# Kernel tuning notes

Hardware: AMD Instinct MI355X
Metric: run time of the kernel (lower is better)

## Reference

```python
import jax, jax.numpy as jnp
import numpy as np

NUM_CLASSES = 20
NUM_ANCHORS = 3
BBOX_ATTRS = 5 + NUM_CLASSES
IMG_H = IMG_W = 416
IN_H = IN_W = 52
CONF_THRES = 0.5
NMS_THRES = 0.4
TOP_K = 2048


def setup_inputs() -> dict:
    key = jax.random.key(0)
    k1, _ = jax.random.split(key)
    inp = jax.random.normal(k1, (16, NUM_ANCHORS * BBOX_ATTRS, IN_H, IN_W), dtype=jnp.float32)
    anchors = jnp.array([[116.0, 90.0], [156.0, 198.0], [373.0, 326.0]], dtype=jnp.float32)
    return {"input": inp, "anchors": anchors}


def decode(inp, anchors):
    """YOLOv3 head decode (YOLOv3Loss.forward with targets=None).
    inp: [B, A*(5+C), H, W] -> output: [B, A*H*W, 5+C] with (cx, cy, w, h, conf, cls...)."""
    bs = inp.shape[0]
    stride_h = IMG_H / IN_H
    stride_w = IMG_W / IN_W
    scaled_anchors = anchors / jnp.array([stride_w, stride_h], dtype=inp.dtype)  # [A, 2]
    # [B, A, H, W, 5+C]
    pred = inp.reshape(bs, NUM_ANCHORS, BBOX_ATTRS, IN_H, IN_W).transpose(0, 1, 3, 4, 2)
    x = jax.nn.sigmoid(pred[..., 0])
    y = jax.nn.sigmoid(pred[..., 1])
    w = pred[..., 2]
    h = pred[..., 3]
    conf = jax.nn.sigmoid(pred[..., 4])
    pred_cls = jax.nn.sigmoid(pred[..., 5:])
    grid_x = jnp.arange(IN_W, dtype=inp.dtype)[None, None, None, :]
    grid_y = jnp.arange(IN_H, dtype=inp.dtype)[None, None, :, None]
    anchor_w = scaled_anchors[:, 0][None, :, None, None]
    anchor_h = scaled_anchors[:, 1][None, :, None, None]
    bx = (x + grid_x) * stride_w
    by = (y + grid_y) * stride_h
    bw = jnp.exp(w) * anchor_w * stride_w
    bh = jnp.exp(h) * anchor_h * stride_h
    boxes = jnp.stack([bx, by, bw, bh], axis=-1).reshape(bs, -1, 4)
    output = jnp.concatenate(
        [boxes, conf.reshape(bs, -1, 1), pred_cls.reshape(bs, -1, NUM_CLASSES)], axis=-1
    )
    return output


def _nms_one(corners, conf, cls_pred):
    """Greedy class-aware NMS over TOP_K conf-sorted candidates.
    corners: [K,4] x1y1x2y2, conf: [K] desc-sorted, cls_pred: [K] int32.
    Returns keep mask [K] bool."""
    x1, y1, x2, y2 = corners[:, 0], corners[:, 1], corners[:, 2], corners[:, 3]
    area = (x2 - x1 + 1.0) * (y2 - y1 + 1.0)
    ix1 = jnp.maximum(x1[:, None], x1[None, :])
    iy1 = jnp.maximum(y1[:, None], y1[None, :])
    ix2 = jnp.minimum(x2[:, None], x2[None, :])
    iy2 = jnp.minimum(y2[:, None], y2[None, :])
    inter = jnp.clip(ix2 - ix1 + 1.0, 0.0) * jnp.clip(iy2 - iy1 + 1.0, 0.0)
    iou = inter / (area[:, None] + area[None, :] - inter + 1e-16)
    # suppress j if kept i (earlier, higher conf, same class) overlaps >= thres
    cond = (iou >= NMS_THRES) & (cls_pred[:, None] == cls_pred[None, :])
    valid = conf >= CONF_THRES
    K = conf.shape[0]
    idx = jnp.arange(K)

    def body(i, carry):
        keep, supp = carry
        ki = valid[i] & (~supp[i])
        keep = keep.at[i].set(ki)
        supp = supp | (cond[i] & (idx > i) & ki)
        return keep, supp

    keep, _ = jax.lax.fori_loop(0, K, body, (jnp.zeros(K, bool), jnp.zeros(K, bool)))
    return keep


def reference(input, anchors):
    output = decode(input, anchors)  # [B, N, 5+C]
    conf = output[..., 4]
    # top-K candidates by objectness (desc order == conf sort in original NMS)
    top_conf, top_idx = jax.lax.top_k(conf, TOP_K)  # [B, K]
    boxes = output[..., :4]
    cx, cy, w, h = boxes[..., 0], boxes[..., 1], boxes[..., 2], boxes[..., 3]
    corners = jnp.stack([cx - w / 2, cy - h / 2, cx + w / 2, cy + h / 2], axis=-1)
    corners_s = jnp.take_along_axis(corners, top_idx[..., None], axis=1)  # [B, K, 4]
    cls_pred = jnp.argmax(output[..., 5:], axis=-1).astype(jnp.int32)  # [B, N]
    cls_s = jnp.take_along_axis(cls_pred, top_idx, axis=1)  # [B, K]
    keep = jax.vmap(_nms_one)(corners_s, top_conf, cls_s)  # [B, K] bool
    return output, top_idx, keep
```

## Files before the change

kernel.cpp:

```cpp
#include <hip/hip_runtime.h>

#pragma clang fp contract(off)

#define B 16
#define A 3
#define HGT 52
#define WID 52
#define HW 2704
#define NCAND 8112
#define CATTR 25
#define TOPK 2048
#define NWORD 64
#define CH 128
#define NCHUNK (TOPK / CH)
#define EPT 8

typedef unsigned int uint32;
typedef unsigned long long u64;

__global__ void decode_kernel(const float* __restrict__ inp,
                              const float* __restrict__ anchors,
                              float* __restrict__ out,
                              float* __restrict__ cws) {
    int t = blockIdx.x * blockDim.x + threadIdx.x;
    if (t >= B * NCAND) return;
    int b  = t / NCAND;
    int n  = t - b * NCAND;
    int a  = n / HW;
    int hw = n - a * HW;
    int gy = hw / WID;
    int gx = hw - gy * WID;
    const float* ip = inp + ((size_t)(b * (A * CATTR) + a * CATTR)) * HW + hw;
    float* op = out + (size_t)t * CATTR;

    float p0 = ip[0 * HW], p1 = ip[1 * HW], p2 = ip[2 * HW], p3 = ip[3 * HW], p4 = ip[4 * HW];
    float sx = 1.0f / (1.0f + expf(-p0));
    float sy = 1.0f / (1.0f + expf(-p1));
    float bx = (sx + (float)gx) * 8.0f;
    float by = (sy + (float)gy) * 8.0f;
    float bw = expf(p2) * anchors[a * 2 + 0];
    float bh = expf(p3) * anchors[a * 2 + 1];
    float cf = 1.0f / (1.0f + expf(-p4));
    op[0] = bx; op[1] = by; op[2] = bw; op[3] = bh; op[4] = cf;
    cws[t] = cf;
#pragma unroll
    for (int c = 0; c < 20; ++c) {
        float v = ip[(5 + c) * HW];
        op[5 + c] = 1.0f / (1.0f + expf(-v));
    }
}

__device__ __forceinline__ void cexd(u64& a, u64& b, bool up) {
    if ((a > b) == up) { u64 tmp = a; a = b; b = tmp; }
}

__device__ __forceinline__ u64 sel(u64 k, u64 o, bool kmin) {
    return kmin ? (k < o ? k : o) : (k > o ? k : o);
}

__device__ __forceinline__ void bitonic_merge_2048(u64 key[EPT], u64* mb, int t) {
    for (unsigned j = 1024; j >= 8; j >>= 1) {
        unsigned m = j >> 3;
        bool kmin = ((t & m) == 0);
        if (m >= 64) {
            __syncthreads();
#pragma unroll
            for (int e = 0; e < EPT; ++e) mb[e * 256 + t] = key[e];
            __syncthreads();
            int pt = t ^ (int)m;
#pragma unroll
            for (int e = 0; e < EPT; ++e) key[e] = sel(key[e], mb[e * 256 + pt], kmin);
        } else {
#pragma unroll
            for (int e = 0; e < EPT; ++e) {
                u64 o = __shfl_xor(key[e], (int)m);
                key[e] = sel(key[e], o, kmin);
            }
        }
    }
    cexd(key[0], key[4], true); cexd(key[1], key[5], true);
    cexd(key[2], key[6], true); cexd(key[3], key[7], true);
    cexd(key[0], key[2], true); cexd(key[1], key[3], true);
    cexd(key[4], key[6], true); cexd(key[5], key[7], true);
    cexd(key[0], key[1], true); cexd(key[2], key[3], true);
    cexd(key[4], key[5], true); cexd(key[6], key[7], true);
}

__global__ __launch_bounds__(256) void sort1_kernel(const float* __restrict__ conf,
                                                    u64* __restrict__ runs) {
    __shared__ u64 mb[2048];
    int blk = blockIdx.x;
    int b = blk >> 2, c = blk & 3;
    int t = threadIdx.x;
    int base = t * EPT;
    int gbase = c * 2048 + base;
    const float* cp = conf + b * NCAND;

    u64 key[EPT];
    if (gbase + EPT <= NCAND) {
        const float4* cp4 = (const float4*)(cp + gbase);
        float4 c0 = cp4[0], c1 = cp4[1];
        float cf[EPT] = {c0.x, c0.y, c0.z, c0.w, c1.x, c1.y, c1.z, c1.w};
#pragma unroll
        for (int e = 0; e < EPT; ++e) {
            unsigned bits = __float_as_uint(cf[e]) | 0x80000000u;
            key[e] = ((u64)(~bits) << 32) | (unsigned)(gbase + e);
        }
    } else {
#pragma unroll
        for (int e = 0; e < EPT; ++e) {
            int idx = gbase + e;
            if (idx < NCAND) {
                unsigned bits = __float_as_uint(cp[idx]) | 0x80000000u;
                key[e] = ((u64)(~bits) << 32) | (unsigned)idx;
            } else key[e] = ~0ull;
        }
    }

    cexd(key[0], key[1], true); cexd(key[2], key[3], false);
    cexd(key[4], key[5], true); cexd(key[6], key[7], false);

    cexd(key[0], key[2], true);  cexd(key[1], key[3], true);
    cexd(key[4], key[6], false); cexd(key[5], key[7], false);
    cexd(key[0], key[1], true);  cexd(key[2], key[3], true);
    cexd(key[4], key[5], false); cexd(key[6], key[7], false);

    bool up8 = ((t & 1) == 0);
    cexd(key[0], key[4], up8); cexd(key[1], key[5], up8);
    cexd(key[2], key[6], up8); cexd(key[3], key[7], up8);
    cexd(key[0], key[2], up8); cexd(key[1], key[3], up8);
    cexd(key[4], key[6], up8); cexd(key[5], key[7], up8);
    cexd(key[0], key[1], up8); cexd(key[2], key[3], up8);
    cexd(key[4], key[5], up8); cexd(key[6], key[7], up8);

    for (unsigned k = 16; k <= 2048; k <<= 1) {
        bool up = (((unsigned)base & k) == 0);
        for (unsigned j = k >> 1; j >= 8; j >>= 1) {
            unsigned m = j >> 3;
            bool kmin = (up == ((t & m) == 0));
            if (m >= 64) {
                __syncthreads();
#pragma unroll
                for (int e = 0; e < EPT; ++e) mb[e * 256 + t] = key[e];
                __syncthreads();
                int pt = t ^ (int)m;
#pragma unroll
                for (int e = 0; e < EPT; ++e) key[e] = sel(key[e], mb[e * 256 + pt], kmin);
            } else {
#pragma unroll
                for (int e = 0; e < EPT; ++e) {
                    u64 o = __shfl_xor(key[e], (int)m);
                    key[e] = sel(key[e], o, kmin);
                }
            }
        }
        cexd(key[0], key[4], up); cexd(key[1], key[5], up);
        cexd(key[2], key[6], up); cexd(key[3], key[7], up);
        cexd(key[0], key[2], up); cexd(key[1], key[3], up);
        cexd(key[4], key[6], up); cexd(key[5], key[7], up);
        cexd(key[0], key[1], up); cexd(key[2], key[3], up);
        cexd(key[4], key[5], up); cexd(key[6], key[7], up);
    }

    u64* R = runs + ((size_t)b * 4 + c) * 2048;
#pragma unroll
    for (int e = 0; e < EPT; ++e) R[base + e] = key[e];
}

__global__ __launch_bounds__(256) void sort2_kernel(const u64* __restrict__ runs,
                                                    u64* __restrict__ half) {
    __shared__ u64 mb[2048];
    int blk = blockIdx.x;
    int b = blk >> 1, p = blk & 1;
    int t = threadIdx.x;
    int base = t * EPT;
    const u64* Av = runs + ((size_t)b * 4 + p * 2) * 2048;
    const u64* Bv = Av + 2048;

    u64 key[EPT];
#pragma unroll
    for (int e = 0; e < EPT; ++e) {
        u64 a = Av[base + e];
        u64 o = Bv[2047 - (base + e)];
        key[e] = a < o ? a : o;
    }
    bitonic_merge_2048(key, mb, t);
    u64* H = half + ((size_t)b * 2 + p) * 2048;
#pragma unroll
    for (int e = 0; e < EPT; ++e) H[base + e] = key[e];
}

__global__ __launch_bounds__(256) void sort3_kernel(const u64* __restrict__ half,
                                                    float* __restrict__ topf) {
    __shared__ u64 mb[2048];
    int b = blockIdx.x;
    int t = threadIdx.x;
    int base = t * EPT;
    const u64* Av = half + (size_t)b * 2 * 2048;
    const u64* Bv = Av + 2048;

    u64 key[EPT];
#pragma unroll
    for (int e = 0; e < EPT; ++e) {
        u64 a = Av[base + e];
        u64 o = Bv[2047 - (base + e)];
        key[e] = a < o ? a : o;
    }
    bitonic_merge_2048(key, mb, t);
#pragma unroll
    for (int e = 0; e < EPT; ++e)
        topf[(size_t)b * TOPK + base + e] = (float)(unsigned)(key[e] & 0xFFFFFFFFu);
}

__global__ __launch_bounds__(256) void geo_kernel(const float* __restrict__ out,
                                                  const float* __restrict__ topf,
                                                  float* __restrict__ gx1,
                                                  float* __restrict__ gy1,
                                                  float* __restrict__ gx2,
                                                  float* __restrict__ gy2,
                                                  float* __restrict__ gar,
                                                  uint32* __restrict__ gcv,
                                                  uint32* __restrict__ vwords) {
    int t = blockIdx.x * blockDim.x + threadIdx.x;
    if (t >= B * TOPK) return;
    int b = t >> 11;
    int r = t & (TOPK - 1);
    int idx = (int)topf[(size_t)b * TOPK + r];
    const float* p = out + ((size_t)b * NCAND + idx) * CATTR;
    float cx = p[0], cy = p[1], w = p[2], h = p[3], cf = p[4];
    float hw_ = w * 0.5f, hh_ = h * 0.5f;
    float x1 = cx - hw_, y1 = cy - hh_, x2 = cx + hw_, y2 = cy + hh_;
    gx1[t] = x1; gy1[t] = y1; gx2[t] = x2; gy2[t] = y2;
    gar[t] = ((x2 - x1) + 1.0f) * ((y2 - y1) + 1.0f);
    float best = p[5]; int bc = 0;
#pragma unroll
    for (int c = 1; c < 20; ++c) {
        float v = p[5 + c];
        if (v > best) { best = v; bc = c; }
    }
    bool valid = (cf >= 0.5f);
    gcv[t] = (uint32)bc | (valid ? 0x100u : 0u);
    unsigned long long bal = __ballot(valid);
    if ((t & 63) == 0) {
        vwords[(t >> 5) + 0] = (uint32)bal;
        vwords[(t >> 5) + 1] = (uint32)(bal >> 32);
    }
}

#define KMID (13421772.5 / 33554432.0)
__global__ __launch_bounds__(1024) void build_kernel(const float* __restrict__ gx1,
                                                     const float* __restrict__ gy1,
                                                     const float* __restrict__ gx2,
                                                     const float* __restrict__ gy2,
                                                     const float* __restrict__ gar,
                                                     const uint32* __restrict__ gcv,
                                                     uint32* __restrict__ rowmask) {
    __shared__ float4 x4s[TOPK];
    __shared__ float  ars[TOPK];
    __shared__ uint32 clss[TOPK];
    int bt   = blockIdx.y;
    int pr   = blockIdx.x;
    int tid  = threadIdx.x;
    int lane = tid & 63;
    int wvq  = tid >> 6;
    int base = bt * TOPK;
    u64* rm64 = (u64*)(rowmask + (size_t)base * NWORD);

    for (int j = tid; j < TOPK; j += 1024) {
        int g = base + j;
        x4s[j]  = make_float4(gx1[g], gy1[g], gx2[g], gy2[g]);
        ars[j]  = gar[g];
        clss[j] = gcv[g] & 0xffu;
    }
    __syncthreads();

#pragma unroll
    for (int s = 0; s < 2; ++s) {
        int r = s ? (31 - pr) : pr;
        int i0 = r * 64 + wvq * 4;
        float4 rq[4]; float rar4[4]; uint32 rcl4[4];
#pragma unroll
        for (int k = 0; k < 4; ++k) {
            rq[k] = x4s[i0 + k]; rar4[k] = ars[i0 + k]; rcl4[k] = clss[i0 + k];
        }
        for (int cg = r; cg < 32; ++cg) {
            int j = cg * 64 + lane;
            float4 c  = x4s[j];
            float car = ars[j];
            uint32 cc = clss[j];
            u64 bal[4];
#pragma unroll
            for (int k = 0; k < 4; ++k) {
                float ix1 = fmaxf(rq[k].x, c.x);
                float iy1 = fmaxf(rq[k].y, c.y);
                float ix2 = fminf(rq[k].z, c.z);
                float iy2 = fminf(rq[k].w, c.w);
                float iw = fmaxf((ix2 - ix1) + 1.0f, 0.0f);
                float ih = fmaxf((iy2 - iy1) + 1.0f, 0.0f);
                float inter = iw * ih;
                float denom = ((rar4[k] + car) - inter) + 1e-16f;
                bool cond = ((double)inter > KMID * (double)denom) && (cc == rcl4[k]);
                bal[k] = __ballot(cond);
            }
            u64 v = bal[0];
            if (lane == 1) v = bal[1];
            if (lane == 2) v = bal[2];
            if (lane == 3) v = bal[3];
            if (lane < 4) rm64[(size_t)(i0 + lane) * 32 + cg] = v;
        }
    }
}

#define SPF 8
__global__ __launch_bounds__(1024) void scan_kernel(const uint32* __restrict__ rowmask,
                                                    const uint32* __restrict__ vwords,
                                                    float* __restrict__ keepf) {
    __shared__ uint32 buf[2][CH * NWORD];
    int bt  = blockIdx.x;
    int tid = threadIdx.x;
    int wv  = tid >> 6;
    int l   = tid & 63;
    const uint32* rm = rowmask + (size_t)bt * TOPK * NWORD;

    if (wv > 0) {
        int ctid = tid - 64;
        const uint4* src = (const uint4*)rm;
        uint4* dst = (uint4*)buf[0];
        for (int o = ctid; o < CH * NWORD / 4; o += 960) dst[o] = src[o];
    }
    uint32 vw = 0, supp = 0, keepw = 0, cur = 0, vcur = 0;
    if (wv == 0) vw = vwords[bt * 64 + l];
    __syncthreads();

    for (int c = 0; c < NCHUNK; ++c) {
        if (wv > 0) {
            if (c + 1 < NCHUNK) {
                int ctid = tid - 64;
                const uint4* src = (const uint4*)(rm + (size_t)(c + 1) * CH * NWORD);
                uint4* dst = (uint4*)buf[(c + 1) & 1];
                for (int o = ctid; o < CH * NWORD / 4; o += 960) dst[o] = src[o];
            }
        } else {
            const uint32* bp = buf[c & 1];
            uint32 rlb[SPF], rwb[SPF];
#pragma unroll
            for (int k = 0; k < SPF; ++k) {
                rlb[k] = bp[k * NWORD + l];
                rwb[k] = bp[k * NWORD + ((c * CH + k) >> 5)];
            }
            for (int kk = 0; kk < CH; kk += SPF) {
#pragma unroll
                for (int k2 = 0; k2 < SPF; ++k2) {
                    int k = kk + k2;
                    int i = c * CH + k;
                    uint32 rl = rlb[k2], rw = rwb[k2];
                    int nk = k + SPF;
                    if (nk < CH) {
                        rlb[k2] = bp[nk * NWORD + l];
                        rwb[k2] = bp[nk * NWORD + ((c * CH + nk) >> 5)];
                    }
                    int b2 = i & 31;
                    if (b2 == 0) {
                        cur  = __shfl(supp, i >> 5);
                        vcur = __shfl(vw,   i >> 5);
                    }
                    uint32 kf = ((vcur >> b2) & ~(cur >> b2)) & 1u;
                    uint32 m = (uint32)(-(int)kf);
                    cur  |= rw & m;
                    supp |= rl & m;
                    if (l == (i >> 5)) keepw |= kf << b2;
                }
            }
        }
        __syncthreads();
    }

    if (wv == 0) {
#pragma unroll
        for (int k = 0; k < 32; ++k)
            keepf[bt * TOPK + l * 32 + k] = (float)((keepw >> k) & 1u);
    }
}

extern "C" void kernel_launch(void* const* d_in, const int* in_sizes, int n_in,
                              void* d_out, int out_size, void* d_ws, size_t ws_size,
                              hipStream_t stream) {
    const float* inp     = (const float*)d_in[0];
    const float* anchors = (const float*)d_in[1];
    float* out   = (float*)d_out;
    float* topf  = out  + (size_t)B * NCAND * CATTR;
    float* keepf = topf + (size_t)B * TOPK;

    float*  cws = (float*)d_ws;
    float*  gx1 = cws + B * NCAND;
    float*  gy1 = gx1 + B * TOPK;
    float*  gx2 = gy1 + B * TOPK;
    float*  gy2 = gx2 + B * TOPK;
    float*  gar = gy2 + B * TOPK;
    uint32* gcv = (uint32*)(gar + B * TOPK);
    uint32* rowmask = gcv + B * TOPK;
    uint32* vwords  = rowmask + (size_t)B * TOPK * NWORD;
    u64* runs = (u64*)rowmask;
    u64* half = runs + (size_t)B * 4 * 2048;

    int total = B * NCAND;
    decode_kernel<<<(total + 255) / 256, 256, 0, stream>>>(inp, anchors, out, cws);
    sort1_kernel<<<B * 4, 256, 0, stream>>>(cws, runs);
    sort2_kernel<<<B * 2, 256, 0, stream>>>(runs, half);
    sort3_kernel<<<B, 256, 0, stream>>>(half, topf);
    geo_kernel<<<(B * TOPK + 255) / 256, 256, 0, stream>>>(out, topf, gx1, gy1, gx2, gy2, gar, gcv, vwords);
    build_kernel<<<dim3(16, B), 1024, 0, stream>>>(gx1, gy1, gx2, gy2, gar, gcv, rowmask);
    scan_kernel<<<B, 1024, 0, stream>>>(rowmask, vwords, keepf);
}
```

Measured before the change: 206.5 us.

## Coalesce decode stores via LDS, fuse geo into sort3, restructure NMS scan

The decode kernel stages each block's 25-attribute rows in shared memory and writes them out as coalesced float4 stores instead of strided per-thread stores. The geometry/class gather is folded into the final sort merge kernel, which removes one launch and the topf round-trip. The NMS scan now resolves 32 candidates at a time within a word using a register-resident diagonal, then ORs in the suppression rows of kept boxes only. This replaces the per-row serial shuffle loop, with a larger chunk size. Fusing geo into sort3 leaves only 16 blocks doing the gathers, so that work runs with much less parallelism than before.

Measured after the change: 257.3 us. +24.6%, slower.

```diff
diff --git a/kernel.cpp b/kernel.cpp
--- a/kernel.cpp
+++ b/kernel.cpp
@@ -11,19 +11,21 @@
 #define CATTR 25
 #define TOPK 2048
 #define NWORD 64
-#define CH 128
+#define CH 256
 #define NCHUNK (TOPK / CH)
+#define GPC (CH / 32)
 #define EPT 8
 
 typedef unsigned int uint32;
 typedef unsigned long long u64;
 
-__global__ void decode_kernel(const float* __restrict__ inp,
-                              const float* __restrict__ anchors,
-                              float* __restrict__ out,
-                              float* __restrict__ cws) {
-    int t = blockIdx.x * blockDim.x + threadIdx.x;
-    if (t >= B * NCAND) return;
+__global__ __launch_bounds__(256) void decode_kernel(const float* __restrict__ inp,
+                                                     const float* __restrict__ anchors,
+                                                     float* __restrict__ out,
+                                                     float* __restrict__ cws) {
+    __shared__ float sm[256 * CATTR];
+    int tid = threadIdx.x;
+    int t = blockIdx.x * 256 + tid;
     int b  = t / NCAND;
     int n  = t - b * NCAND;
     int a  = n / HW;
@@ -31,7 +33,7 @@
     int gy = hw / WID;
     int gx = hw - gy * WID;
     const float* ip = inp + ((size_t)(b * (A * CATTR) + a * CATTR)) * HW + hw;
-    float* op = out + (size_t)t * CATTR;
+    float* sp = sm + tid * CATTR;
 
     float p0 = ip[0 * HW], p1 = ip[1 * HW], p2 = ip[2 * HW], p3 = ip[3 * HW], p4 = ip[4 * HW];
     float sx = 1.0f / (1.0f + expf(-p0));
@@ -41,13 +43,19 @@
     float bw = expf(p2) * anchors[a * 2 + 0];
     float bh = expf(p3) * anchors[a * 2 + 1];
     float cf = 1.0f / (1.0f + expf(-p4));
-    op[0] = bx; op[1] = by; op[2] = bw; op[3] = bh; op[4] = cf;
+    sp[0] = bx; sp[1] = by; sp[2] = bw; sp[3] = bh; sp[4] = cf;
     cws[t] = cf;
 #pragma unroll
     for (int c = 0; c < 20; ++c) {
         float v = ip[(5 + c) * HW];
-        op[5 + c] = 1.0f / (1.0f + expf(-v));
-    }
+        sp[5 + c] = 1.0f / (1.0f + expf(-v));
+    }
+    __syncthreads();
+    const float4* sm4 = (const float4*)sm;
+    float4* o4 = (float4*)(out + (size_t)blockIdx.x * 256 * CATTR);
+#pragma unroll
+    for (int k = 0; k < 6; ++k) o4[k * 256 + tid] = sm4[k * 256 + tid];
+    if (tid < 64) o4[1536 + tid] = sm4[1536 + tid];
 }
 
 __device__ __forceinline__ void cexd(u64& a, u64& b, bool up) {
@@ -191,8 +199,17 @@
 }
 
 __global__ __launch_bounds__(256) void sort3_kernel(const u64* __restrict__ half,
-                                                    float* __restrict__ topf) {
+                                                    const float* __restrict__ out,
+                                                    float* __restrict__ topf,
+                                                    float* __restrict__ gx1,
+                                                    float* __restrict__ gy1,
+                                                    float* __restrict__ gx2,
+                                                    float* __restrict__ gy2,
+                                                    float* __restrict__ gar,
+                                                    uint32* __restrict__ gcv,
+                                                    uint32* __restrict__ vwords) {
     __shared__ u64 mb[2048];
+    __shared__ uint32 vb[256];
     int b = blockIdx.x;
     int t = threadIdx.x;
     int base = t * EPT;
@@ -207,43 +224,34 @@
         key[e] = a < o ? a : o;
     }
     bitonic_merge_2048(key, mb, t);
-#pragma unroll
-    for (int e = 0; e < EPT; ++e)
-        topf[(size_t)b * TOPK + base + e] = (float)(unsigned)(key[e] & 0xFFFFFFFFu);
-}
-
-__global__ __launch_bounds__(256) void geo_kernel(const float* __restrict__ out,
-                                                  const float* __restrict__ topf,
-                                                  float* __restrict__ gx1,
-                                                  float* __restrict__ gy1,
-                                                  float* __restrict__ gx2,
-                                                  float* __restrict__ gy2,
-                                                  float* __restrict__ gar,
-                                                  uint32* __restrict__ gcv,
-                                                  uint32* __restrict__ vwords) {
-    int t = blockIdx.x * blockDim.x + threadIdx.x;
-    if (t >= B * TOPK) return;
-    int b = t >> 11;
-    int r = t & (TOPK - 1);
-    int idx = (int)topf[(size_t)b * TOPK + r];
-    const float* p = out + ((size_t)b * NCAND + idx) * CATTR;
-    float cx = p[0], cy = p[1], w = p[2], h = p[3], cf = p[4];
-    float hw_ = w * 0.5f, hh_ = h * 0.5f;
-    float x1 = cx - hw_, y1 = cy - hh_, x2 = cx + hw_, y2 = cy + hh_;
-    gx1[t] = x1; gy1[t] = y1; gx2[t] = x2; gy2[t] = y2;
-    gar[t] = ((x2 - x1) + 1.0f) * ((y2 - y1) + 1.0f);
-    float best = p[5]; int bc = 0;
-#pragma unroll
-    for (int c = 1; c < 20; ++c) {
-        float v = p[5 + c];
-        if (v > best) { best = v; bc = c; }
-    }
-    bool valid = (cf >= 0.5f);
-    gcv[t] = (uint32)bc | (valid ? 0x100u : 0u);
-    unsigned long long bal = __ballot(valid);
-    if ((t & 63) == 0) {
-        vwords[(t >> 5) + 0] = (uint32)bal;
-        vwords[(t >> 5) + 1] = (uint32)(bal >> 32);
+
+    const float* ob = out + (size_t)b * NCAND * CATTR;
+    uint32 vbits = 0;
+#pragma unroll
+    for (int e = 0; e < EPT; ++e) {
+        uint32 idx = (uint32)(key[e] & 0xFFFFFFFFu);
+        int tg = b * TOPK + base + e;
+        topf[tg] = (float)idx;
+        const float* p = ob + (size_t)idx * CATTR;
+        float cx = p[0], cy = p[1], w = p[2], h = p[3], cf = p[4];
+        float hw_ = w * 0.5f, hh_ = h * 0.5f;
+        float x1 = cx - hw_, y1 = cy - hh_, x2 = cx + hw_, y2 = cy + hh_;
+        gx1[tg] = x1; gy1[tg] = y1; gx2[tg] = x2; gy2[tg] = y2;
+        gar[tg] = ((x2 - x1) + 1.0f) * ((y2 - y1) + 1.0f);
+        float best = p[5]; int bc = 0;
+#pragma unroll
+        for (int c = 1; c < 20; ++c) {
+            float v = p[5 + c];
+            if (v > best) { best = v; bc = c; }
+        }
+        gcv[tg] = (uint32)bc;
+        vbits |= (cf >= 0.5f ? 1u : 0u) << e;
+    }
+    vb[t] = vbits;
+    __syncthreads();
+    if (t < 64) {
+        uint32 w4 = vb[t * 4] | (vb[t * 4 + 1] << 8) | (vb[t * 4 + 2] << 16) | (vb[t * 4 + 3] << 24);
+        vwords[b * 64 + t] = w4;
     }
 }
 
@@ -311,7 +319,6 @@
     }
 }
 
-#define SPF 8
 __global__ __launch_bounds__(1024) void scan_kernel(const uint32* __restrict__ rowmask,
                                                     const uint32* __restrict__ vwords,
                                                     float* __restrict__ keepf) {
@@ -328,8 +335,8 @@
         uint4* dst = (uint4*)buf[0];
         for (int o = ctid; o < CH * NWORD / 4; o += 960) dst[o] = src[o];
     }
-    uint32 vw = 0, supp = 0, keepw = 0, cur = 0, vcur = 0;
-    if (wv == 0) vw = vwords[bt * 64 + l];
+    uint32 supp = 0, keepw = 0;
+    if (wv == 0) supp = ~vwords[bt * 64 + l];
     __syncthreads();
 
     for (int c = 0; c < NCHUNK; ++c) {
@@ -342,34 +349,30 @@
             }
         } else {
             const uint32* bp = buf[c & 1];
-            uint32 rlb[SPF], rwb[SPF];
-#pragma unroll
-            for (int k = 0; k < SPF; ++k) {
-                rlb[k] = bp[k * NWORD + l];
-                rwb[k] = bp[k * NWORD + ((c * CH + k) >> 5)];
-            }
-            for (int kk = 0; kk < CH; kk += SPF) {
-#pragma unroll
-                for (int k2 = 0; k2 < SPF; ++k2) {
-                    int k = kk + k2;
-                    int i = c * CH + k;
-                    uint32 rl = rlb[k2], rw = rwb[k2];
-                    int nk = k + SPF;
-                    if (nk < CH) {
-                        rlb[k2] = bp[nk * NWORD + l];
-                        rwb[k2] = bp[nk * NWORD + ((c * CH + nk) >> 5)];
-                    }
-                    int b2 = i & 31;
-                    if (b2 == 0) {
-                        cur  = __shfl(supp, i >> 5);
-                        vcur = __shfl(vw,   i >> 5);
-                    }
-                    uint32 kf = ((vcur >> b2) & ~(cur >> b2)) & 1u;
-                    uint32 m = (uint32)(-(int)kf);
-                    cur  |= rw & m;
-                    supp |= rl & m;
-                    if (l == (i >> 5)) keepw |= kf << b2;
+            uint32 sw[32];
+#pragma unroll
+            for (int k = 0; k < 32; ++k) sw[k] = bp[k * NWORD + c * GPC];
+            for (int gl = 0; gl < GPC; ++gl) {
+                int g = c * GPC + gl;
+                uint32 cur = __shfl(supp, g);
+                uint32 keep = 0;
+#pragma unroll
+                for (int k = 0; k < 32; ++k) {
+                    uint32 bitk = (cur >> k) & 1u;
+                    keep |= (bitk ^ 1u) << k;
+                    cur |= sw[k] & (bitk - 1u);
                 }
+                if (l == g) keepw = keep;
+                if (gl + 1 < GPC) {
+#pragma unroll
+                    for (int k = 0; k < 32; ++k) sw[k] = bp[((gl + 1) * 32 + k) * NWORD + (g + 1)];
+                }
+                uint32 rows = keep, upd = 0;
+                while (rows) {
+                    int k = __builtin_ctz(rows); rows &= rows - 1;
+                    upd |= bp[(gl * 32 + k) * NWORD + l];
+                }
+                supp |= upd;
             }
         }
         __syncthreads();
@@ -403,12 +406,10 @@
     u64* runs = (u64*)rowmask;
     u64* half = runs + (size_t)B * 4 * 2048;
 
-    int total = B * NCAND;
-    decode_kernel<<<(total + 255) / 256, 256, 0, stream>>>(inp, anchors, out, cws);
+    decode_kernel<<<(B * NCAND) / 256, 256, 0, stream>>>(inp, anchors, out, cws);
     sort1_kernel<<<B * 4, 256, 0, stream>>>(cws, runs);
     sort2_kernel<<<B * 2, 256, 0, stream>>>(runs, half);
-    sort3_kernel<<<B, 256, 0, stream>>>(half, topf);
-    geo_kernel<<<(B * TOPK + 255) / 256, 256, 0, stream>>>(out, topf, gx1, gy1, gx2, gy2, gar, gcv, vwords);
+    sort3_kernel<<<B, 256, 0, stream>>>(half, out, topf, gx1, gy1, gx2, gy2, gar, gcv, vwords);
     build_kernel<<<dim3(16, B), 1024, 0, stream>>>(gx1, gy1, gx2, gy2, gar, gcv, rowmask);
     scan_kernel<<<B, 1024, 0, stream>>>(rowmask, vwords, keepf);
 }
```
